# Optimization experiments

Hardware: AMD Instinct MI355X
Metric: run time of the kernel (lower is better)

The kernel has to match this reference:

```python
import jax, jax.numpy as jnp
import numpy as np

NUM_HEAD = 32
NUM_KV_HEAD = 8
HEAD_DIM = 128
EMBED_DIM = 4096
GROUP = NUM_HEAD // NUM_KV_HEAD + 2  # 6: 4 q slots + 1 k + 1 v
TOKENS = 64


def setup_inputs() -> dict:
    key = jax.random.key(0)
    k1, k2, k3 = jax.random.split(key, 3)
    inp = jax.random.normal(k1, (TOKENS, EMBED_DIM), dtype=jnp.float32)
    # fused GQA weight layout from load_parameter: [embed_dim, num_kv_head, group, head_dim]
    weight = jax.random.normal(k2, (EMBED_DIM, NUM_KV_HEAD, GROUP, HEAD_DIM), dtype=jnp.float32) * 0.02
    bias = jax.random.normal(k3, (NUM_KV_HEAD, GROUP, HEAD_DIM), dtype=jnp.float32) * 0.02
    return {"input": inp, "weight": weight, "bias": bias}


def reference(input, weight, bias):
    # fused grouped QKV GEMM (mm_qkv_group_out):
    # out[t, kv, g, d] = sum_e input[t, e] * weight[e, kv, g, d] + bias[kv, g, d]
    out = jnp.einsum('te,ekgd->tkgd', input, weight) + bias
    T = input.shape[0]
    q = out[:, :, : GROUP - 2, :].reshape(T, NUM_HEAD * HEAD_DIM)
    k = out[:, :, GROUP - 2, :].reshape(T, NUM_KV_HEAD * HEAD_DIM)
    v = out[:, :, GROUP - 1, :].reshape(T, NUM_KV_HEAD * HEAD_DIM)
    return (q, k, v)
```

## Files before the change

### kernel.cpp

```cpp
#include <hip/hip_runtime.h>


#define N_COLS 6144
#define K_DIM  4096
#define Q_SZ   (64 * 4096)
#define K_OFF  Q_SZ
#define V_OFF  (Q_SZ + 64 * 1024)
#define OUT_ELEMS 393216
#define NT     48
#define KSPLIT 16
#define BK     32
#define TILES  8

typedef __bf16 bf16x8 __attribute__((ext_vector_type(8)));
typedef float  f32x4  __attribute__((ext_vector_type(4)));
typedef unsigned int u32x4 __attribute__((ext_vector_type(4)));

__device__ __forceinline__ unsigned short f2bf_rne(float f) {
    unsigned int u = __float_as_uint(f);
    u += 0x7FFFu + ((u >> 16) & 1u);
    return (unsigned short)(u >> 16);
}

__device__ __forceinline__ unsigned int pack_pair(float lo, float hi) {
    return ((unsigned int)f2bf_rne(hi) << 16) | f2bf_rne(lo);
}

__device__ __forceinline__ int out_index(int t, int n) {
    const int kv = n / 768;
    const int g  = (n >> 7) % 6;
    const int d  = n & 127;
    if (g < 4)  return t * 4096 + kv * 512 + g * 128 + d;
    if (g == 4) return K_OFF + t * 1024 + kv * 128 + d;
    return V_OFF + t * 1024 + kv * 128 + d;
}

#define GLDS(gp, lp) __builtin_amdgcn_global_load_lds(                        \
    (const __attribute__((address_space(1))) void*)(gp),                      \
    (__attribute__((address_space(3))) void*)(lp), 16, 0, 0)

__global__ __launch_bounds__(256, 4)
void qkv_gemm(const float* __restrict__ in, const float* __restrict__ w,
              float* __restrict__ part) {
    __shared__ float Ws[BK * 128];

    const int tid  = threadIdx.x;
    const int nt   = blockIdx.x % NT;
    const int kq   = blockIdx.x / NT;
    const int n0   = nt * 128;
    const int k0   = kq * 256;
    const int wid  = tid >> 6;
    const int lane = tid & 63;
    const int l15  = lane & 15;
    const int kblk = lane >> 4;

    f32x4 acc[2][4];
    #pragma unroll
    for (int a = 0; a < 2; ++a)
        #pragma unroll
        for (int b = 0; b < 4; ++b) acc[a][b] = (f32x4){0.f, 0.f, 0.f, 0.f};

    #pragma unroll 1
    for (int s = 0; s < TILES; ++s) {
        const int kc = k0 + s * BK;

        const float* wr = w + (size_t)kc * N_COLS + n0;
        #pragma unroll
        for (int r = 0; r < 4; ++r) {
            const int u = r * 256 + tid;
            GLDS(wr + (size_t)(u >> 5) * N_COLS + (u & 31) * 4, &Ws[u * 4]);
        }

        float4 alo[4], ahi[4];
        #pragma unroll
        for (int mi = 0; mi < 4; ++mi) {
            const float* ap = in + (size_t)(mi * 16 + l15) * K_DIM + kc + kblk * 8;
            alo[mi] = *(const float4*)ap;
            ahi[mi] = *(const float4*)(ap + 4);
        }

        __syncthreads();

        u32x4 af[4];
        #pragma unroll
        for (int mi = 0; mi < 4; ++mi) {
            af[mi][0] = pack_pair(alo[mi].x, alo[mi].y);
            af[mi][1] = pack_pair(alo[mi].z, alo[mi].w);
            af[mi][2] = pack_pair(ahi[mi].x, ahi[mi].y);
            af[mi][3] = pack_pair(ahi[mi].z, ahi[mi].w);
        }

        #pragma unroll
        for (int nfi = 0; nfi < 2; ++nfi) {
            const int nb = (wid * 2 + nfi) * 16 + l15;
            float bf[8];
            #pragma unroll
            for (int j = 0; j < 8; ++j)
                bf[j] = Ws[(kblk * 8 + j) * 128 + nb];
            u32x4 bu;
            #pragma unroll
            for (int j2 = 0; j2 < 4; ++j2)
                bu[j2] = pack_pair(bf[2 * j2], bf[2 * j2 + 1]);

            const bf16x8 bv = __builtin_bit_cast(bf16x8, bu);
            #pragma unroll
            for (int mi = 0; mi < 4; ++mi)
                acc[nfi][mi] = __builtin_amdgcn_mfma_f32_16x16x32_bf16(
                    __builtin_bit_cast(bf16x8, af[mi]), bv, acc[nfi][mi], 0, 0, 0);
        }

        __syncthreads();
    }

    float* pb = part + (size_t)kq * OUT_ELEMS;
    #pragma unroll
    for (int nfi = 0; nfi < 2; ++nfi) {
        const int n = n0 + (wid * 2 + nfi) * 16 + l15;
        #pragma unroll
        for (int mi = 0; mi < 4; ++mi) {
            #pragma unroll
            for (int r = 0; r < 4; ++r) {
                const int t = mi * 16 + kblk * 4 + r;
                pb[(size_t)t * N_COLS + n] = acc[nfi][mi][r];
            }
        }
    }
}

__global__ __launch_bounds__(256)
void qkv_reduce(const float* __restrict__ part, const float* __restrict__ bias,
                float* __restrict__ out) {
    const int i = blockIdx.x * 256 + threadIdx.x;
    const int t = i / N_COLS;
    const int n = i % N_COLS;
    float s = bias[n];
    #pragma unroll
    for (int kq = 0; kq < KSPLIT; ++kq)
        s += part[(size_t)kq * OUT_ELEMS + i];
    out[out_index(t, n)] = s;
}

extern "C" void kernel_launch(void* const* d_in, const int* in_sizes, int n_in,
                              void* d_out, int out_size, void* d_ws, size_t ws_size,
                              hipStream_t stream) {
    const float* in   = (const float*)d_in[0];
    const float* w    = (const float*)d_in[1];
    const float* bias = (const float*)d_in[2];
    float* out  = (float*)d_out;
    float* part = (float*)d_ws;

    qkv_gemm<<<NT * KSPLIT, 256, 0, stream>>>(in, w, part);
    qkv_reduce<<<OUT_ELEMS / 256, 256, 0, stream>>>(part, bias, out);
}
```

Before: 163.4 us.

## Double-buffer weight tiles, swizzle LDS, use native bf16 casts, vectorize reduce

```diff
diff --git a/kernel.cpp b/kernel.cpp
--- a/kernel.cpp
+++ b/kernel.cpp
@@ -14,17 +14,6 @@
 
 typedef __bf16 bf16x8 __attribute__((ext_vector_type(8)));
 typedef float  f32x4  __attribute__((ext_vector_type(4)));
-typedef unsigned int u32x4 __attribute__((ext_vector_type(4)));
-
-__device__ __forceinline__ unsigned short f2bf_rne(float f) {
-    unsigned int u = __float_as_uint(f);
-    u += 0x7FFFu + ((u >> 16) & 1u);
-    return (unsigned short)(u >> 16);
-}
-
-__device__ __forceinline__ unsigned int pack_pair(float lo, float hi) {
-    return ((unsigned int)f2bf_rne(hi) << 16) | f2bf_rne(lo);
-}
 
 __device__ __forceinline__ int out_index(int t, int n) {
     const int kv = n / 768;
@@ -39,16 +28,18 @@
     (const __attribute__((address_space(1))) void*)(gp),                      \
     (__attribute__((address_space(3))) void*)(lp), 16, 0, 0)
 
-__global__ __launch_bounds__(256, 4)
+#define VWAIT4() asm volatile("s_waitcnt vmcnt(4)" ::: "memory")
+
+__global__ __launch_bounds__(256, 3)
 void qkv_gemm(const float* __restrict__ in, const float* __restrict__ w,
               float* __restrict__ part) {
-    __shared__ float Ws[BK * 128];
+    __shared__ float Ws[2][BK * 128];
 
     const int tid  = threadIdx.x;
     const int nt   = blockIdx.x % NT;
     const int kq   = blockIdx.x / NT;
     const int n0   = nt * 128;
-    const int k0   = kq * 256;
+    const int k0   = kq * (BK * TILES);
     const int wid  = tid >> 6;
     const int lane = tid & 63;
     const int l15  = lane & 15;
@@ -60,56 +51,69 @@
         #pragma unroll
         for (int b = 0; b < 4; ++b) acc[a][b] = (f32x4){0.f, 0.f, 0.f, 0.f};
 
-    #pragma unroll 1
-    for (int s = 0; s < TILES; ++s) {
+    float4 aloA[4], ahiA[4], aloB[4], ahiB[4];
+
+    auto STAGE = [&](int s, int buf) {
         const int kc = k0 + s * BK;
-
         const float* wr = w + (size_t)kc * N_COLS + n0;
         #pragma unroll
         for (int r = 0; r < 4; ++r) {
             const int u = r * 256 + tid;
-            GLDS(wr + (size_t)(u >> 5) * N_COLS + (u & 31) * 4, &Ws[u * 4]);
+            const int c = (u & 31) ^ (((u >> 8) & 3) << 2);
+            GLDS(wr + (size_t)(u >> 5) * N_COLS + c * 4, &Ws[buf][u * 4]);
         }
+    };
 
-        float4 alo[4], ahi[4];
+    auto LOADA = [&](int s, float4 (&alo)[4], float4 (&ahi)[4]) {
+        const int kc = k0 + s * BK;
         #pragma unroll
         for (int mi = 0; mi < 4; ++mi) {
             const float* ap = in + (size_t)(mi * 16 + l15) * K_DIM + kc + kblk * 8;
             alo[mi] = *(const float4*)ap;
             ahi[mi] = *(const float4*)(ap + 4);
         }
+    };
 
-        __syncthreads();
-
-        u32x4 af[4];
+    auto BODY = [&](const float4 (&alo)[4], const float4 (&ahi)[4], int buf) {
+        bf16x8 av[4];
         #pragma unroll
         for (int mi = 0; mi < 4; ++mi) {
-            af[mi][0] = pack_pair(alo[mi].x, alo[mi].y);
-            af[mi][1] = pack_pair(alo[mi].z, alo[mi].w);
-            af[mi][2] = pack_pair(ahi[mi].x, ahi[mi].y);
-            af[mi][3] = pack_pair(ahi[mi].z, ahi[mi].w);
+            av[mi][0] = (__bf16)alo[mi].x; av[mi][1] = (__bf16)alo[mi].y;
+            av[mi][2] = (__bf16)alo[mi].z; av[mi][3] = (__bf16)alo[mi].w;
+            av[mi][4] = (__bf16)ahi[mi].x; av[mi][5] = (__bf16)ahi[mi].y;
+            av[mi][6] = (__bf16)ahi[mi].z; av[mi][7] = (__bf16)ahi[mi].w;
         }
-
         #pragma unroll
         for (int nfi = 0; nfi < 2; ++nfi) {
-            const int nb = (wid * 2 + nfi) * 16 + l15;
-            float bf[8];
+            const int nb   = (wid * 2 + nfi) * 16 + l15;
+            const int base = kblk * 1024 + (nb ^ (kblk << 4));
+            bf16x8 bv;
             #pragma unroll
             for (int j = 0; j < 8; ++j)
-                bf[j] = Ws[(kblk * 8 + j) * 128 + nb];
-            u32x4 bu;
-            #pragma unroll
-            for (int j2 = 0; j2 < 4; ++j2)
-                bu[j2] = pack_pair(bf[2 * j2], bf[2 * j2 + 1]);
-
-            const bf16x8 bv = __builtin_bit_cast(bf16x8, bu);
+                bv[j] = (__bf16)Ws[buf][base + j * 128];
             #pragma unroll
             for (int mi = 0; mi < 4; ++mi)
                 acc[nfi][mi] = __builtin_amdgcn_mfma_f32_16x16x32_bf16(
-                    __builtin_bit_cast(bf16x8, af[mi]), bv, acc[nfi][mi], 0, 0, 0);
+                    av[mi], bv, acc[nfi][mi], 0, 0, 0);
         }
+    };
 
-        __syncthreads();
+    STAGE(0, 0);
+    LOADA(0, aloA, ahiA);
+
+    #pragma unroll
+    for (int s = 0; s < TILES; ++s) {
+        if (s + 1 < TILES) STAGE(s + 1, (s + 1) & 1);
+        VWAIT4();
+        __builtin_amdgcn_s_barrier();
+        if ((s & 1) == 0) {
+            if (s + 1 < TILES) LOADA(s + 1, aloB, ahiB);
+            BODY(aloA, ahiA, 0);
+        } else {
+            if (s + 1 < TILES) LOADA(s + 1, aloA, ahiA);
+            BODY(aloB, ahiB, 1);
+        }
+        __builtin_amdgcn_s_barrier();
     }
 
     float* pb = part + (size_t)kq * OUT_ELEMS;
@@ -130,14 +134,14 @@
 __global__ __launch_bounds__(256)
 void qkv_reduce(const float* __restrict__ part, const float* __restrict__ bias,
                 float* __restrict__ out) {
-    const int i = blockIdx.x * 256 + threadIdx.x;
+    const int i = (blockIdx.x * 256 + threadIdx.x) << 2;
     const int t = i / N_COLS;
-    const int n = i % N_COLS;
-    float s = bias[n];
+    const int n = i - t * N_COLS;
+    f32x4 s = *(const f32x4*)(bias + n);
     #pragma unroll
     for (int kq = 0; kq < KSPLIT; ++kq)
-        s += part[(size_t)kq * OUT_ELEMS + i];
-    out[out_index(t, n)] = s;
+        s += *(const f32x4*)(part + (size_t)kq * OUT_ELEMS + i);
+    *(f32x4*)(out + out_index(t, n)) = s;
 }
 
 extern "C" void kernel_launch(void* const* d_in, const int* in_sizes, int n_in,
@@ -150,5 +154,5 @@
     float* part = (float*)d_ws;
 
     qkv_gemm<<<NT * KSPLIT, 256, 0, stream>>>(in, w, part);
-    qkv_reduce<<<OUT_ELEMS / 256, 256, 0, stream>>>(part, bias, out);
+    qkv_reduce<<<OUT_ELEMS / 1024, 256, 0, stream>>>(part, bias, out);
 }
```

New measurement: 162.7 us. Within noise of the previous version (-0.5%).
